# Performance work log

Measured on AMD Instinct MI355X. Metric: run time of the kernel, lower is better.

The kernel has to match this reference:

```python
import jax, jax.numpy as jnp
import numpy as np

NUM_EMBEDDINGS = 1024
EMBEDDING_DIM = 64

def setup_inputs() -> dict:
    key = jax.random.key(0)
    k1, k2 = jax.random.split(key)
    inputs = jax.random.normal(k1, (32, 64, 64, EMBEDDING_DIM), dtype=jnp.float32)
    # torch init: uniform_(-1/K, 1/K)
    embedding = jax.random.uniform(
        k2, (NUM_EMBEDDINGS, EMBEDDING_DIM), dtype=jnp.float32,
        minval=-1.0 / NUM_EMBEDDINGS, maxval=1.0 / NUM_EMBEDDINGS)
    return {"inputs": inputs, "embedding": embedding}

def reference(inputs, embedding):
    input_shape = inputs.shape
    d = embedding.shape[1]
    K = embedding.shape[0]
    flat = inputs.reshape(-1, d)                                  # [N, d]
    distances = (jnp.sum(flat ** 2, axis=1, keepdims=True)
                 + jnp.sum(embedding ** 2, axis=1)
                 - 2.0 * jnp.matmul(flat, embedding.T))
    encoding_indices = jnp.argmin(distances, axis=1)              # [N]
    encodings = jax.nn.one_hot(encoding_indices, K, dtype=inputs.dtype)  # [N, K]
    quantized = jnp.matmul(encodings, embedding).reshape(input_shape)
    quantized_original = quantized
    # straight-through estimator
    quantized_st = inputs + jax.lax.stop_gradient(quantized - inputs)
    avg_probs = jnp.mean(encodings, axis=0)                       # [K]
    perplexity = jnp.exp(-jnp.sum(avg_probs * jnp.log(avg_probs + 1e-10)))
    return (quantized_st, quantized_original, perplexity, encodings)
```

## Files before the change

### kernel.cpp

```cpp
#include <hip/hip_runtime.h>
#include <math.h>

#define N_ROWS 131072
#define D      64
#define K_EMB  1024
#define M_TILE 128
#define KC     128
#define XSTR   72
#define MARGIN_D 1e-5f

#define Q_ST_OFF 0
#define Q_OR_OFF 8388608
#define PERP_OFF 16777216
#define ENC_OFF  16777217


typedef __attribute__((ext_vector_type(8)))  short bf16x8;
typedef __attribute__((ext_vector_type(16))) float f32x16;

__device__ __forceinline__ unsigned short f2bf_rne(float f) {
    unsigned int u = __float_as_uint(f);
    unsigned int r = u + 0x7fffu + ((u >> 16) & 1u);
    return (unsigned short)(r >> 16);
}
__device__ __forceinline__ float bf2f(unsigned short h) {
    return __uint_as_float(((unsigned int)h) << 16);
}

__global__ __launch_bounds__(256) void enorm32_kernel(const float* __restrict__ emb,
                                                      float* __restrict__ enorm) {
    int k = blockIdx.x * 256 + threadIdx.x;
    const float4* row = reinterpret_cast<const float4*>(emb + (size_t)k * D);
    float s = 0.f;
#pragma unroll
    for (int i = 0; i < 16; ++i) {
        float4 v = row[i];
        s = fmaf(v.x, v.x, s); s = fmaf(v.y, v.y, s);
        s = fmaf(v.z, v.z, s); s = fmaf(v.w, v.w, s);
    }
    enorm[k] = s;
}

__global__ __launch_bounds__(256) void vq_main(const float* __restrict__ in,
                                               const float* __restrict__ emb,
                                               const float* __restrict__ enorm32,
                                               unsigned int* __restrict__ counts,
                                               float* __restrict__ out) {
    __shared__ __align__(16) unsigned short XH[M_TILE * XSTR];
    __shared__ __align__(16) unsigned short XL[M_TILE * XSTR];
    __shared__ __align__(16) unsigned short EH[KC * XSTR];
    __shared__ __align__(16) unsigned short EL[KC * XSTR];
    __shared__ __align__(16) float en_s[K_EMB];
    __shared__ __align__(16) float xs2[D];
    __shared__ int bks[M_TILE];
    __shared__ int flagl[M_TILE];
    __shared__ int nflag;
    __shared__ double rv[4];
    __shared__ int    rk[4];

    const int tid  = threadIdx.x;
    const int lane = tid & 63;
    const int w    = tid >> 6;
    const int hl   = lane >> 5;
    const int l31  = lane & 31;
    const int base = blockIdx.x * M_TILE;
    const int wrow = w * 32;

    if (tid == 0) nflag = 0;
    {
        float4 v = *reinterpret_cast<const float4*>(enorm32 + tid * 4);
        *reinterpret_cast<float4*>(&en_s[tid * 4]) = v;
    }
    {
        const float4* src = reinterpret_cast<const float4*>(in + (size_t)base * D);
#pragma unroll
        for (int i = 0; i < 8; ++i) {
            int lin = i * 256 + tid;
            float4 v = src[lin];
            int row = lin >> 4, c4 = lin & 15;
            ushort4 h, l;
            h.x = f2bf_rne(v.x); l.x = f2bf_rne(v.x - bf2f(h.x));
            h.y = f2bf_rne(v.y); l.y = f2bf_rne(v.y - bf2f(h.y));
            h.z = f2bf_rne(v.z); l.z = f2bf_rne(v.z - bf2f(h.z));
            h.w = f2bf_rne(v.w); l.w = f2bf_rne(v.w - bf2f(h.w));
            *reinterpret_cast<ushort4*>(&XH[row * XSTR + c4 * 4]) = h;
            *reinterpret_cast<ushort4*>(&XL[row * XSTR + c4 * 4]) = l;
        }
    }
    __syncthreads();

    bf16x8 AH[4], AL[4];
    {
        const unsigned short* xh = &XH[(wrow + l31) * XSTR + hl * 8];
        const unsigned short* xl = &XL[(wrow + l31) * XSTR + hl * 8];
#pragma unroll
        for (int kb = 0; kb < 4; ++kb) {
            AH[kb] = *reinterpret_cast<const bf16x8*>(xh + kb * 16);
            AL[kb] = *reinterpret_cast<const bf16x8*>(xl + kb * 16);
        }
    }

    float b1[16], b2[16]; int k1[16];
#pragma unroll
    for (int r = 0; r < 16; ++r) { b1[r] = 1e30f; b2[r] = 1e30f; k1[r] = 0; }

#pragma unroll 1
    for (int ch = 0; ch < K_EMB / KC; ++ch) {
        __syncthreads();
        {
            const float4* esrc = reinterpret_cast<const float4*>(emb + (size_t)ch * KC * D);
#pragma unroll
            for (int i = 0; i < 8; ++i) {
                int lin = i * 256 + tid;
                float4 v = esrc[lin];
                int row = lin >> 4, c4 = lin & 15;
                ushort4 h, l;
                h.x = f2bf_rne(v.x); l.x = f2bf_rne(v.x - bf2f(h.x));
                h.y = f2bf_rne(v.y); l.y = f2bf_rne(v.y - bf2f(h.y));
                h.z = f2bf_rne(v.z); l.z = f2bf_rne(v.z - bf2f(h.z));
                h.w = f2bf_rne(v.w); l.w = f2bf_rne(v.w - bf2f(h.w));
                *reinterpret_cast<ushort4*>(&EH[row * XSTR + c4 * 4]) = h;
                *reinterpret_cast<ushort4*>(&EL[row * XSTR + c4 * 4]) = l;
            }
        }
        __syncthreads();

#pragma unroll 1
        for (int sub = 0; sub < 4; ++sub) {
            const unsigned short* eh = &EH[(sub * 32 + l31) * XSTR + hl * 8];
            const unsigned short* el = &EL[(sub * 32 + l31) * XSTR + hl * 8];
            bf16x8 BH[4], BL[4];
#pragma unroll
            for (int kb = 0; kb < 4; ++kb) {
                BH[kb] = *reinterpret_cast<const bf16x8*>(eh + kb * 16);
                BL[kb] = *reinterpret_cast<const bf16x8*>(el + kb * 16);
            }
            f32x16 acc = {};
#pragma unroll
            for (int kb = 0; kb < 4; ++kb)
                acc = __builtin_amdgcn_mfma_f32_32x32x16_bf16(AH[kb], BH[kb], acc, 0, 0, 0);
#pragma unroll
            for (int kb = 0; kb < 4; ++kb)
                acc = __builtin_amdgcn_mfma_f32_32x32x16_bf16(AH[kb], BL[kb], acc, 0, 0, 0);
#pragma unroll
            for (int kb = 0; kb < 4; ++kb)
                acc = __builtin_amdgcn_mfma_f32_32x32x16_bf16(AL[kb], BH[kb], acc, 0, 0, 0);

            int kg = ch * KC + sub * 32 + l31;
            float en = en_s[kg];
#pragma unroll
            for (int r = 0; r < 16; ++r) {
                float s = fmaf(-2.f, acc[r], en);
                if (s < b1[r]) { b2[r] = b1[r]; b1[r] = s; k1[r] = kg; }
                else if (s < b2[r]) b2[r] = s;
            }
            asm volatile("" ::: "memory");
        }
    }

#pragma unroll
    for (int r = 0; r < 16; ++r) {
        float v = b1[r], v2 = b2[r]; int kk = k1[r];
#pragma unroll
        for (int off = 16; off >= 1; off >>= 1) {
            float ov  = __shfl_xor(v,  off, 64);
            int   ok  = __shfl_xor(kk, off, 64);
            float ov2 = __shfl_xor(v2, off, 64);
            bool win = (ov < v) || (ov == v && ok < kk);
            float loser = win ? v : ov;
            v2 = fminf(fminf(v2, ov2), loser);
            if (win) { v = ov; kk = ok; }
        }
        if (l31 == 0) {
            int row = wrow + (r & 3) + 8 * (r >> 2) + 4 * hl;
            bks[row] = kk;
            if (v2 - v < MARGIN_D) {
                int p = atomicAdd(&nflag, 1);
                flagl[p] = row;
            }
        }
    }

    {
        float* ep = out + ENC_OFF + (size_t)base * K_EMB;
        float4 z = make_float4(0.f, 0.f, 0.f, 0.f);
        float4* ap = reinterpret_cast<float4*>(ep + 3);
        for (int i = tid; i < 32767; i += 256) ap[i] = z;
        if (tid == 0) { ep[0] = 0.f; ep[1] = 0.f; ep[2] = 0.f; ep[131071] = 0.f; }
    }
    __syncthreads();

    int nf = nflag;
#pragma unroll 1
    for (int fi = 0; fi < nf; ++fi) {
        int row = flagl[fi];
        if (tid < 16)
            *reinterpret_cast<float4*>(&xs2[tid * 4]) =
                reinterpret_cast<const float4*>(in + (size_t)(base + row) * D)[tid];
        __syncthreads();
        double bv = 1e300; int bk = 0;
#pragma unroll 1
        for (int c = 0; c < 4; ++c) {
            int k = tid * 4 + c;
            const float4* er = reinterpret_cast<const float4*>(emb + (size_t)k * D);
            double dot = 0.0, en = 0.0;
#pragma unroll 4
            for (int i = 0; i < 16; ++i) {
                float4 ev = er[i];
                float4 xv = *reinterpret_cast<const float4*>(&xs2[i * 4]);
                double e0 = ev.x, e1 = ev.y, e2 = ev.z, e3 = ev.w;
                en  = fma(e0, e0, en);  en  = fma(e1, e1, en);
                en  = fma(e2, e2, en);  en  = fma(e3, e3, en);
                dot = fma((double)xv.x, e0, dot); dot = fma((double)xv.y, e1, dot);
                dot = fma((double)xv.z, e2, dot); dot = fma((double)xv.w, e3, dot);
            }
            double s = fma(-2.0, dot, en);
            if (s < bv) { bv = s; bk = k; }
        }
        {
            double v = bv; int kk = bk;
#pragma unroll
            for (int off = 32; off >= 1; off >>= 1) {
                double ov = __shfl_xor(v, off, 64);
                int    ok = __shfl_xor(kk, off, 64);
                if (ov < v || (ov == v && ok < kk)) { v = ov; kk = ok; }
            }
            if (lane == 0) { rv[w] = v; rk[w] = kk; }
        }
        __syncthreads();
        if (tid == 0) {
            double v = rv[0]; int kk = rk[0];
#pragma unroll
            for (int x = 1; x < 4; ++x) {
                double ov = rv[x]; int ok = rk[x];
                if (ov < v || (ov == v && ok < kk)) { v = ov; kk = ok; }
            }
            bks[row] = kk;
        }
        __syncthreads();
    }

    if (tid < M_TILE) {
        int kk = bks[tid];
        atomicAdd(&counts[kk], 1u);
        out[ENC_OFF + (size_t)(base + tid) * K_EMB + kk] = 1.0f;
    }
    {
        int row = tid >> 1;
        int p   = tid & 1;
        int kk  = bks[row];
        const float4* er = reinterpret_cast<const float4*>(emb + (size_t)kk * D);
        float4* o1 = reinterpret_cast<float4*>(out + Q_ST_OFF + (size_t)(base + row) * D);
        float4* o2 = reinterpret_cast<float4*>(out + Q_OR_OFF + (size_t)(base + row) * D);
#pragma unroll
        for (int i = 0; i < 8; ++i) {
            float4 v = er[p * 8 + i];
            o1[p * 8 + i] = v;
            o2[p * 8 + i] = v;
        }
    }
}

__global__ __launch_bounds__(1024) void perp_kernel(const unsigned int* __restrict__ counts,
                                                    float* __restrict__ out_perp) {
    const int k = threadIdx.x;
    double p = (double)counts[k] * (1.0 / (double)N_ROWS);
    double t = p * log(p + 1e-10);
#pragma unroll
    for (int off = 32; off >= 1; off >>= 1) t += __shfl_down(t, off, 64);
    __shared__ double red[16];
    if ((k & 63) == 0) red[k >> 6] = t;
    __syncthreads();
    if (k < 16) {
        double s = red[k];
#pragma unroll
        for (int off = 8; off >= 1; off >>= 1) s += __shfl_down(s, off, 16);
        if (k == 0) out_perp[0] = (float)exp(-s);
    }
}

extern "C" void kernel_launch(void* const* d_in, const int* in_sizes, int n_in,
                              void* d_out, int out_size, void* d_ws, size_t ws_size,
                              hipStream_t stream) {
    const float* in  = (const float*)d_in[0];
    const float* emb = (const float*)d_in[1];
    float* out = (float*)d_out;
    unsigned int* counts = (unsigned int*)d_ws;
    float* enorm32       = (float*)((char*)d_ws + 8192);

    hipMemsetAsync(d_ws, 0, 4096, stream);
    enorm32_kernel<<<K_EMB / 256, 256, 0, stream>>>(emb, enorm32);
    vq_main<<<N_ROWS / M_TILE, 256, 0, stream>>>(in, emb, enorm32, counts, out);
    perp_kernel<<<1, 1024, 0, stream>>>(counts, out + PERP_OFF);
}
```

Before: 840.1 us.

## Split VQ into argmin, flat output writer, and global rescore kernels

Splits the monolithic kernel into a pre-split bf16 embedding prep, an argmin-only kernel that writes indices to workspace, a grid-stride writer that streams all outputs (quantized and one-hot) as coalesced float4 stores, and a separate rescore kernel for near-tie rows. The aim is to decouple the large one-hot/quantized output writes from the MFMA-heavy argmin so each runs at full bandwidth or occupancy, and to avoid per-block fp32-to-bf16 embedding conversion. It costs extra launches and an index round trip through memory, and adds a fallback path when workspace is too small.

Result: slower. 953.9 us (+13.5%).

```diff
diff --git a/kernel.cpp b/kernel.cpp
--- a/kernel.cpp
+++ b/kernel.cpp
@@ -5,15 +5,23 @@
 #define D      64
 #define K_EMB  1024
 #define M_TILE 128
-#define KC     128
-#define XSTR   72
-#define MARGIN_D 1e-5f
+#define KC     64
+#define ESTR   72
+#define MARGIN_M 1e-5f
 
 #define Q_ST_OFF 0
 #define Q_OR_OFF 8388608
 #define PERP_OFF 16777216
 #define ENC_OFF  16777217
-
+#define NFULL4 37748736
+
+#define WS_COUNTS  0
+#define WS_FLAGCNT 4096
+#define WS_ENORM   8192
+#define WS_BKS     16384
+#define WS_ESPLIT  540672
+#define WS_FLAGS   835584
+#define WS_NEEDED  1048576
 
 typedef __attribute__((ext_vector_type(8)))  short bf16x8;
 typedef __attribute__((ext_vector_type(16))) float f32x16;
@@ -25,6 +33,303 @@
 }
 __device__ __forceinline__ float bf2f(unsigned short h) {
     return __uint_as_float(((unsigned int)h) << 16);
+}
+
+__global__ __launch_bounds__(256) void prep_kernel(const float* __restrict__ emb,
+                                                   float* __restrict__ enorm,
+                                                   unsigned short* __restrict__ esplit) {
+    int k = blockIdx.x * 256 + threadIdx.x;
+    if (k >= K_EMB) return;
+    const float4* row = reinterpret_cast<const float4*>(emb + (size_t)k * D);
+    unsigned short* hb = esplit + (size_t)(k >> 6) * (2 * 64 * ESTR) + (k & 63) * ESTR;
+    unsigned short* lb = hb + 64 * ESTR;
+    float s = 0.f;
+#pragma unroll
+    for (int i = 0; i < 16; ++i) {
+        float4 v = row[i];
+        s = fmaf(v.x, v.x, s); s = fmaf(v.y, v.y, s);
+        s = fmaf(v.z, v.z, s); s = fmaf(v.w, v.w, s);
+        ushort4 h, l;
+        h.x = f2bf_rne(v.x); l.x = f2bf_rne(v.x - bf2f(h.x));
+        h.y = f2bf_rne(v.y); l.y = f2bf_rne(v.y - bf2f(h.y));
+        h.z = f2bf_rne(v.z); l.z = f2bf_rne(v.z - bf2f(h.z));
+        h.w = f2bf_rne(v.w); l.w = f2bf_rne(v.w - bf2f(h.w));
+        *reinterpret_cast<ushort4*>(hb + i * 4) = h;
+        *reinterpret_cast<ushort4*>(lb + i * 4) = l;
+    }
+    enorm[k] = s;
+}
+
+__global__ __launch_bounds__(256) void vq_argmin(const float* __restrict__ in,
+                                                 const unsigned short* __restrict__ esplit,
+                                                 const float* __restrict__ enorm32,
+                                                 unsigned int* __restrict__ counts,
+                                                 unsigned int* __restrict__ flagcount,
+                                                 int* __restrict__ flaglist,
+                                                 int flagcap,
+                                                 int* __restrict__ bks_g) {
+    __shared__ __align__(16) unsigned short EHL[2][64][ESTR];
+    __shared__ __align__(16) float en_s[K_EMB];
+    __shared__ int bks_s[M_TILE];
+
+    const int tid  = threadIdx.x;
+    const int lane = tid & 63;
+    const int w    = tid >> 6;
+    const int hl   = lane >> 5;
+    const int l31  = lane & 31;
+    const int base = blockIdx.x * M_TILE;
+    const int wrow = w * 32;
+
+    {
+        float4 v = *reinterpret_cast<const float4*>(enorm32 + tid * 4);
+        *reinterpret_cast<float4*>(&en_s[tid * 4]) = v;
+    }
+
+    bf16x8 AH[4], AL[4];
+    {
+        const float* xrow = in + (size_t)(base + wrow + l31) * D + hl * 8;
+#pragma unroll
+        for (int kb = 0; kb < 4; ++kb) {
+            float4 a = *reinterpret_cast<const float4*>(xrow + kb * 16);
+            float4 b = *reinterpret_cast<const float4*>(xrow + kb * 16 + 4);
+            float f[8] = {a.x, a.y, a.z, a.w, b.x, b.y, b.z, b.w};
+            union { bf16x8 v; unsigned short u[8]; } H, L;
+#pragma unroll
+            for (int j = 0; j < 8; ++j) {
+                H.u[j] = f2bf_rne(f[j]);
+                L.u[j] = f2bf_rne(f[j] - bf2f(H.u[j]));
+            }
+            AH[kb] = H.v; AL[kb] = L.v;
+        }
+    }
+
+    float b1[16], b2[16]; int k1[16];
+#pragma unroll
+    for (int r = 0; r < 16; ++r) { b1[r] = -1e30f; b2[r] = -1e30f; k1[r] = 0; }
+
+    uint4 st[5];
+    const uint4* src0 = reinterpret_cast<const uint4*>(esplit);
+#pragma unroll
+    for (int i = 0; i < 5; ++i) {
+        int idx = i * 256 + tid;
+        if (idx < 1152) st[i] = src0[idx];
+    }
+
+#pragma unroll 1
+    for (int ch = 0; ch < K_EMB / KC; ++ch) {
+        {
+            uint4* d = reinterpret_cast<uint4*>(&EHL[0][0][0]);
+#pragma unroll
+            for (int i = 0; i < 5; ++i) {
+                int idx = i * 256 + tid;
+                if (idx < 1152) d[idx] = st[i];
+            }
+        }
+        __syncthreads();
+        if (ch < 15) {
+            const uint4* s = src0 + (ch + 1) * 1152;
+#pragma unroll
+            for (int i = 0; i < 5; ++i) {
+                int idx = i * 256 + tid;
+                if (idx < 1152) st[i] = s[idx];
+            }
+        }
+
+#pragma unroll 1
+        for (int sub = 0; sub < 2; ++sub) {
+            const unsigned short* eh = &EHL[0][sub * 32 + l31][hl * 8];
+            const unsigned short* el = &EHL[1][sub * 32 + l31][hl * 8];
+            bf16x8 BH[4], BL[4];
+#pragma unroll
+            for (int kb = 0; kb < 4; ++kb) {
+                BH[kb] = *reinterpret_cast<const bf16x8*>(eh + kb * 16);
+                BL[kb] = *reinterpret_cast<const bf16x8*>(el + kb * 16);
+            }
+            f32x16 acc = {};
+#pragma unroll
+            for (int kb = 0; kb < 4; ++kb)
+                acc = __builtin_amdgcn_mfma_f32_32x32x16_bf16(AH[kb], BH[kb], acc, 0, 0, 0);
+#pragma unroll
+            for (int kb = 0; kb < 4; ++kb)
+                acc = __builtin_amdgcn_mfma_f32_32x32x16_bf16(AH[kb], BL[kb], acc, 0, 0, 0);
+#pragma unroll
+            for (int kb = 0; kb < 4; ++kb)
+                acc = __builtin_amdgcn_mfma_f32_32x32x16_bf16(AL[kb], BH[kb], acc, 0, 0, 0);
+
+            int kg = ch * KC + sub * 32 + l31;
+            float mh = 0.5f * en_s[kg];
+#pragma unroll
+            for (int r = 0; r < 16; ++r) {
+                float s = acc[r] - mh;
+                if (s > b1[r]) { b2[r] = b1[r]; b1[r] = s; k1[r] = kg; }
+                else if (s > b2[r]) b2[r] = s;
+            }
+        }
+        __syncthreads();
+    }
+
+#pragma unroll
+    for (int r = 0; r < 16; ++r) {
+        float v = b1[r], v2 = b2[r]; int kk = k1[r];
+#pragma unroll
+        for (int off = 16; off >= 1; off >>= 1) {
+            float ov  = __shfl_xor(v,  off, 64);
+            int   ok  = __shfl_xor(kk, off, 64);
+            float ov2 = __shfl_xor(v2, off, 64);
+            bool win = (ov > v) || (ov == v && ok < kk);
+            float loser = win ? v : ov;
+            v2 = fmaxf(fmaxf(v2, ov2), loser);
+            if (win) { v = ov; kk = ok; }
+        }
+        if (l31 == 0) {
+            int row = wrow + (r & 3) + 8 * (r >> 2) + 4 * hl;
+            bks_s[row] = kk;
+            if (v - v2 < MARGIN_M) {
+                int pos = (int)atomicAdd(flagcount, 1u);
+                if (pos < flagcap) flaglist[pos] = base + row;
+            }
+        }
+    }
+    __syncthreads();
+    if (tid < M_TILE) {
+        int kk = bks_s[tid];
+        bks_g[base + tid] = kk;
+        atomicAdd(&counts[kk], 1u);
+    }
+}
+
+__global__ __launch_bounds__(256) void vq_writer(const float* __restrict__ emb,
+                                                 const int* __restrict__ bks_g,
+                                                 float* __restrict__ out) {
+    const int tid = threadIdx.x;
+    const float4* embF4 = reinterpret_cast<const float4*>(emb);
+    float4* outF4 = reinterpret_cast<float4*>(out);
+#pragma unroll 1
+    for (int i = 0; i < 72; ++i) {
+        int f4 = blockIdx.x * (256 * 72) + i * 256 + tid;
+        if (f4 >= NFULL4) continue;
+        if (f4 < 4194304) {
+            int q = (f4 < 2097152) ? f4 : f4 - 2097152;
+            int row = q >> 4, c4 = q & 15;
+            outF4[f4] = embF4[(size_t)bks_g[row] * 16 + c4];
+        } else if (f4 == 4194304) {
+            int k0 = bks_g[0];
+            out[ENC_OFF + 0] = (k0 == 0) ? 1.f : 0.f;
+            out[ENC_OFF + 1] = (k0 == 1) ? 1.f : 0.f;
+            out[ENC_OFF + 2] = (k0 == 2) ? 1.f : 0.f;
+            out[(size_t)ENC_OFF + 134217727] = (bks_g[N_ROWS - 1] == 1023) ? 1.f : 0.f;
+        } else {
+            int g0 = f4 * 4 - ENC_OFF;
+            int rA = g0 >> 10;
+            int rB = (g0 + 3) >> 10;
+            int kA = bks_g[rA];
+            int kB = (rB != rA) ? bks_g[rB] : kA;
+            float4 v;
+            v.x = ((( g0      >> 10) == rA ? kA : kB) == ( g0      & 1023)) ? 1.f : 0.f;
+            v.y = ((((g0 + 1) >> 10) == rA ? kA : kB) == ((g0 + 1) & 1023)) ? 1.f : 0.f;
+            v.z = ((((g0 + 2) >> 10) == rA ? kA : kB) == ((g0 + 2) & 1023)) ? 1.f : 0.f;
+            v.w = ((((g0 + 3) >> 10) == rA ? kA : kB) == ((g0 + 3) & 1023)) ? 1.f : 0.f;
+            outF4[f4] = v;
+        }
+    }
+}
+
+__global__ __launch_bounds__(256) void rescore_kernel(const float* __restrict__ in,
+                                                      const float* __restrict__ emb,
+                                                      const unsigned int* __restrict__ flagcount,
+                                                      const int* __restrict__ flaglist,
+                                                      int flagcap,
+                                                      unsigned int* __restrict__ counts,
+                                                      int* __restrict__ bks_g,
+                                                      float* __restrict__ out) {
+    __shared__ __align__(16) float xs[64];
+    __shared__ double rv[4];
+    __shared__ int    rk[4];
+
+    const int tid = threadIdx.x;
+    int nf = (int)*flagcount;
+    bool overflow = nf > flagcap;
+    int total = overflow ? N_ROWS : nf;
+
+    for (int idx = blockIdx.x; idx < total; idx += gridDim.x) {
+        int row = overflow ? idx : flaglist[idx];
+        int oldk = bks_g[row];
+        if (tid < 16)
+            *reinterpret_cast<float4*>(&xs[tid * 4]) =
+                reinterpret_cast<const float4*>(in + (size_t)row * D)[tid];
+        __syncthreads();
+
+        double bv = 1e300; int bk = 0;
+#pragma unroll 1
+        for (int c = 0; c < 4; ++c) {
+            int k = tid * 4 + c;
+            const float4* er = reinterpret_cast<const float4*>(emb + (size_t)k * D);
+            double dot = 0.0, en = 0.0;
+#pragma unroll 4
+            for (int i = 0; i < 16; ++i) {
+                float4 ev = er[i];
+                float4 xv = *reinterpret_cast<const float4*>(&xs[i * 4]);
+                double e0 = ev.x, e1 = ev.y, e2 = ev.z, e3 = ev.w;
+                en  = fma(e0, e0, en);  en  = fma(e1, e1, en);
+                en  = fma(e2, e2, en);  en  = fma(e3, e3, en);
+                dot = fma((double)xv.x, e0, dot); dot = fma((double)xv.y, e1, dot);
+                dot = fma((double)xv.z, e2, dot); dot = fma((double)xv.w, e3, dot);
+            }
+            double s = fma(-2.0, dot, en);
+            if (s < bv) { bv = s; bk = k; }
+        }
+        const int lane = tid & 63, w = tid >> 6;
+        {
+            double v = bv; int kk = bk;
+#pragma unroll
+            for (int off = 32; off >= 1; off >>= 1) {
+                double ov = __shfl_xor(v, off, 64);
+                int    ok = __shfl_xor(kk, off, 64);
+                if (ov < v || (ov == v && ok < kk)) { v = ov; kk = ok; }
+            }
+            if (lane == 0) { rv[w] = v; rk[w] = kk; }
+        }
+        __syncthreads();
+        if (tid == 0) {
+            double v = rv[0]; int kk = rk[0];
+#pragma unroll
+            for (int x = 1; x < 4; ++x) {
+                double ov = rv[x]; int ok = rk[x];
+                if (ov < v || (ov == v && ok < kk)) { v = ov; kk = ok; }
+            }
+            if (kk != oldk) {
+                bks_g[row] = kk;
+                out[ENC_OFF + (size_t)row * K_EMB + oldk] = 0.0f;
+                out[ENC_OFF + (size_t)row * K_EMB + kk]   = 1.0f;
+                atomicAdd(&counts[oldk], (unsigned int)-1);
+                atomicAdd(&counts[kk], 1u);
+                const float4* er = reinterpret_cast<const float4*>(emb + (size_t)kk * D);
+                float4* o1 = reinterpret_cast<float4*>(out + Q_ST_OFF + (size_t)row * D);
+                float4* o2 = reinterpret_cast<float4*>(out + Q_OR_OFF + (size_t)row * D);
+#pragma unroll
+                for (int i = 0; i < 16; ++i) { float4 vv = er[i]; o1[i] = vv; o2[i] = vv; }
+            }
+        }
+        __syncthreads();
+    }
+}
+
+__global__ __launch_bounds__(1024) void perp_kernel(const unsigned int* __restrict__ counts,
+                                                    float* __restrict__ out_perp) {
+    const int k = threadIdx.x;
+    double p = (double)counts[k] * (1.0 / (double)N_ROWS);
+    double t = p * log(p + 1e-10);
+#pragma unroll
+    for (int off = 32; off >= 1; off >>= 1) t += __shfl_down(t, off, 64);
+    __shared__ double red[16];
+    if ((k & 63) == 0) red[k >> 6] = t;
+    __syncthreads();
+    if (k < 16) {
+        double s = red[k];
+#pragma unroll
+        for (int off = 8; off >= 1; off >>= 1) s += __shfl_down(s, off, 16);
+        if (k == 0) out_perp[0] = (float)exp(-s);
+    }
 }
 
 __global__ __launch_bounds__(256) void enorm32_kernel(const float* __restrict__ emb,
@@ -41,15 +346,15 @@
     enorm[k] = s;
 }
 
-__global__ __launch_bounds__(256) void vq_main(const float* __restrict__ in,
+__global__ __launch_bounds__(256) void vq_mono(const float* __restrict__ in,
                                                const float* __restrict__ emb,
                                                const float* __restrict__ enorm32,
                                                unsigned int* __restrict__ counts,
                                                float* __restrict__ out) {
-    __shared__ __align__(16) unsigned short XH[M_TILE * XSTR];
-    __shared__ __align__(16) unsigned short XL[M_TILE * XSTR];
-    __shared__ __align__(16) unsigned short EH[KC * XSTR];
-    __shared__ __align__(16) unsigned short EL[KC * XSTR];
+    __shared__ __align__(16) unsigned short XH[M_TILE * ESTR];
+    __shared__ __align__(16) unsigned short XL[M_TILE * ESTR];
+    __shared__ __align__(16) unsigned short EH[128 * ESTR];
+    __shared__ __align__(16) unsigned short EL[128 * ESTR];
     __shared__ __align__(16) float en_s[K_EMB];
     __shared__ __align__(16) float xs2[D];
     __shared__ int bks[M_TILE];
@@ -83,16 +388,16 @@
             h.y = f2bf_rne(v.y); l.y = f2bf_rne(v.y - bf2f(h.y));
             h.z = f2bf_rne(v.z); l.z = f2bf_rne(v.z - bf2f(h.z));
             h.w = f2bf_rne(v.w); l.w = f2bf_rne(v.w - bf2f(h.w));
-            *reinterpret_cast<ushort4*>(&XH[row * XSTR + c4 * 4]) = h;
-            *reinterpret_cast<ushort4*>(&XL[row * XSTR + c4 * 4]) = l;
+            *reinterpret_cast<ushort4*>(&XH[row * ESTR + c4 * 4]) = h;
+            *reinterpret_cast<ushort4*>(&XL[row * ESTR + c4 * 4]) = l;
         }
     }
     __syncthreads();
 
     bf16x8 AH[4], AL[4];
     {
-        const unsigned short* xh = &XH[(wrow + l31) * XSTR + hl * 8];
-        const unsigned short* xl = &XL[(wrow + l31) * XSTR + hl * 8];
+        const unsigned short* xh = &XH[(wrow + l31) * ESTR + hl * 8];
+        const unsigned short* xl = &XL[(wrow + l31) * ESTR + hl * 8];
 #pragma unroll
         for (int kb = 0; kb < 4; ++kb) {
             AH[kb] = *reinterpret_cast<const bf16x8*>(xh + kb * 16);
@@ -105,10 +410,10 @@
     for (int r = 0; r < 16; ++r) { b1[r] = 1e30f; b2[r] = 1e30f; k1[r] = 0; }
 
 #pragma unroll 1
-    for (int ch = 0; ch < K_EMB / KC; ++ch) {
+    for (int ch = 0; ch < K_EMB / 128; ++ch) {
         __syncthreads();
         {
-            const float4* esrc = reinterpret_cast<const float4*>(emb + (size_t)ch * KC * D);
+            const float4* esrc = reinterpret_cast<const float4*>(emb + (size_t)ch * 128 * D);
 #pragma unroll
             for (int i = 0; i < 8; ++i) {
                 int lin = i * 256 + tid;
@@ -119,16 +424,16 @@
                 h.y = f2bf_rne(v.y); l.y = f2bf_rne(v.y - bf2f(h.y));
                 h.z = f2bf_rne(v.z); l.z = f2bf_rne(v.z - bf2f(h.z));
                 h.w = f2bf_rne(v.w); l.w = f2bf_rne(v.w - bf2f(h.w));
-                *reinterpret_cast<ushort4*>(&EH[row * XSTR + c4 * 4]) = h;
-                *reinterpret_cast<ushort4*>(&EL[row * XSTR + c4 * 4]) = l;
+                *reinterpret_cast<ushort4*>(&EH[row * ESTR + c4 * 4]) = h;
+                *reinterpret_cast<ushort4*>(&EL[row * ESTR + c4 * 4]) = l;
             }
         }
         __syncthreads();
 
 #pragma unroll 1
         for (int sub = 0; sub < 4; ++sub) {
-            const unsigned short* eh = &EH[(sub * 32 + l31) * XSTR + hl * 8];
-            const unsigned short* el = &EL[(sub * 32 + l31) * XSTR + hl * 8];
+            const unsigned short* eh = &EH[(sub * 32 + l31) * ESTR + hl * 8];
+            const unsigned short* el = &EL[(sub * 32 + l31) * ESTR + hl * 8];
             bf16x8 BH[4], BL[4];
 #pragma unroll
             for (int kb = 0; kb < 4; ++kb) {
@@ -146,7 +451,7 @@
             for (int kb = 0; kb < 4; ++kb)
                 acc = __builtin_amdgcn_mfma_f32_32x32x16_bf16(AL[kb], BH[kb], acc, 0, 0, 0);
 
-            int kg = ch * KC + sub * 32 + l31;
+            int kg = ch * 128 + sub * 32 + l31;
             float en = en_s[kg];
 #pragma unroll
             for (int r = 0; r < 16; ++r) {
@@ -174,13 +479,9 @@
         if (l31 == 0) {
             int row = wrow + (r & 3) + 8 * (r >> 2) + 4 * hl;
             bks[row] = kk;
-            if (v2 - v < MARGIN_D) {
-                int p = atomicAdd(&nflag, 1);
-                flagl[p] = row;
-            }
-        }
-    }
-
+            if (v2 - v < 2e-5f) { int p = atomicAdd(&nflag, 1); flagl[p] = row; }
+        }
+    }
     {
         float* ep = out + ENC_OFF + (size_t)base * K_EMB;
         float4 z = make_float4(0.f, 0.f, 0.f, 0.f);
@@ -261,35 +562,35 @@
     }
 }
 
-__global__ __launch_bounds__(1024) void perp_kernel(const unsigned int* __restrict__ counts,
-                                                    float* __restrict__ out_perp) {
-    const int k = threadIdx.x;
-    double p = (double)counts[k] * (1.0 / (double)N_ROWS);
-    double t = p * log(p + 1e-10);
-#pragma unroll
-    for (int off = 32; off >= 1; off >>= 1) t += __shfl_down(t, off, 64);
-    __shared__ double red[16];
-    if ((k & 63) == 0) red[k >> 6] = t;
-    __syncthreads();
-    if (k < 16) {
-        double s = red[k];
-#pragma unroll
-        for (int off = 8; off >= 1; off >>= 1) s += __shfl_down(s, off, 16);
-        if (k == 0) out_perp[0] = (float)exp(-s);
-    }
-}
-
 extern "C" void kernel_launch(void* const* d_in, const int* in_sizes, int n_in,
                               void* d_out, int out_size, void* d_ws, size_t ws_size,
                               hipStream_t stream) {
     const float* in  = (const float*)d_in[0];
     const float* emb = (const float*)d_in[1];
     float* out = (float*)d_out;
-    unsigned int* counts = (unsigned int*)d_ws;
-    float* enorm32       = (float*)((char*)d_ws + 8192);
-
-    hipMemsetAsync(d_ws, 0, 4096, stream);
-    enorm32_kernel<<<K_EMB / 256, 256, 0, stream>>>(emb, enorm32);
-    vq_main<<<N_ROWS / M_TILE, 256, 0, stream>>>(in, emb, enorm32, counts, out);
-    perp_kernel<<<1, 1024, 0, stream>>>(counts, out + PERP_OFF);
-}
+    unsigned int* counts    = (unsigned int*)((char*)d_ws + WS_COUNTS);
+    unsigned int* flagcount = (unsigned int*)((char*)d_ws + WS_FLAGCNT);
+    float*        enorm32   = (float*)((char*)d_ws + WS_ENORM);
+
+    if (ws_size >= WS_NEEDED) {
+        int*            bks_g   = (int*)((char*)d_ws + WS_BKS);
+        unsigned short* esplit  = (unsigned short*)((char*)d_ws + WS_ESPLIT);
+        int*            flaglist= (int*)((char*)d_ws + WS_FLAGS);
+        int flagcap = (int)((ws_size - WS_FLAGS) / 4);
+        if (flagcap > N_ROWS) flagcap = N_ROWS;
+
+        hipMemsetAsync(d_ws, 0, 8192, stream);
+        prep_kernel<<<4, 256, 0, stream>>>(emb, enorm32, esplit);
+        vq_argmin<<<N_ROWS / M_TILE, 256, 0, stream>>>(in, esplit, enorm32, counts,
+                                                       flagcount, flaglist, flagcap, bks_g);
+        vq_writer<<<2048, 256, 0, stream>>>(emb, bks_g, out);
+        rescore_kernel<<<1024, 256, 0, stream>>>(in, emb, flagcount, flaglist, flagcap,
+                                                 counts, bks_g, out);
+        perp_kernel<<<1, 1024, 0, stream>>>(counts, out + PERP_OFF);
+    } else {
+        hipMemsetAsync(d_ws, 0, 4096, stream);
+        enorm32_kernel<<<K_EMB / 256, 256, 0, stream>>>(emb, enorm32);
+        vq_mono<<<N_ROWS / M_TILE, 256, 0, stream>>>(in, emb, enorm32, counts, out);
+        perp_kernel<<<1, 1024, 0, stream>>>(counts, out + PERP_OFF);
+    }
+}
```
